# Performance work log

Hardware: AMD Instinct MI355X
Metric: run time of the kernel (lower is better)

The kernel has to match this reference:

```python
import jax, jax.numpy as jnp
import numpy as np

U, N, E, D = 200000, 50000, 1600000, 64


def setup_inputs() -> dict:
    key = jax.random.key(0)
    ks = jax.random.split(key, 8)
    nodes = jax.random.randint(ks[0], (N,), 0, U)
    neigh_idx = jax.random.randint(ks[1], (E,), 0, U)
    seg_ids = jnp.sort(jax.random.randint(ks[2], (E,), 0, N))
    u2e = jax.random.normal(ks[3], (U, D), dtype=jnp.float32) * 0.1
    W1 = jax.random.normal(ks[4], (2 * D, D), dtype=jnp.float32) * 0.1
    b1 = jnp.zeros((D,), dtype=jnp.float32)
    W2 = jax.random.normal(ks[5], (D, D), dtype=jnp.float32) * 0.1
    b2 = jnp.zeros((D,), dtype=jnp.float32)
    w3 = jax.random.normal(ks[6], (D, 1), dtype=jnp.float32) * 0.1
    b3 = jnp.zeros((1,), dtype=jnp.float32)
    return {"nodes": nodes, "neigh_idx": neigh_idx, "seg_ids": seg_ids,
            "u2e": u2e, "W1": W1, "b1": b1, "W2": W2, "b2": b2,
            "w3": w3, "b3": b3}


def reference(nodes, neigh_idx, seg_ids, u2e, W1, b1, W2, b2, w3, b3):
    # Per-node self representation  [N, D]
    u_rep = u2e[nodes]
    # Ragged neighbor gather flattened to edge list
    e_u = u2e[neigh_idx]                      # [E, D]
    u_edge = u_rep[seg_ids]                   # [E, D] node rep broadcast to its edges
    # Attention MLP (GraphRec-style), eval mode (no dropout)
    x = jnp.concatenate([e_u, u_edge], axis=1)            # [E, 2D]
    x = jax.nn.relu(x @ W1 + b1)
    x = jax.nn.relu(x @ W2 + b2)
    logits = (x @ w3 + b3)[:, 0]                           # [E]
    # Segment softmax over each node's neighbor set
    seg_max = jax.ops.segment_max(logits, seg_ids, num_segments=N)
    ex = jnp.exp(logits - seg_max[seg_ids])
    denom = jax.ops.segment_sum(ex, seg_ids, num_segments=N)
    att = ex / denom[seg_ids]                              # [E]
    # Attention-weighted neighbor aggregation: e_u^T @ att per node
    agg = jax.ops.segment_sum(att[:, None] * e_u, seg_ids, num_segments=N)  # [N, D]
    # Nodes with zero neighbors fall back to their own embedding
    counts = jax.ops.segment_sum(jnp.ones((E,), dtype=jnp.float32), seg_ids, num_segments=N)
    out = jnp.where(counts[:, None] > 0, agg, u_rep)
    return out
```

## Files before the change

### kernel.cpp

```cpp
#include <hip/hip_runtime.h>
#include <math.h>

#define D 64

typedef __fp16 fp16x2 __attribute__((ext_vector_type(2)));
typedef _Float16 half8 __attribute__((ext_vector_type(8)));
typedef _Float16 half4v __attribute__((ext_vector_type(4)));
typedef __attribute__((ext_vector_type(4))) float f32x4;

union h8pun { half8 v; fp16x2 h2[4]; };

__global__ __launch_bounds__(256) void k_prep(const float* __restrict__ W1,
                                              const float* __restrict__ W2,
                                              float* __restrict__ W1at,
                                              float* __restrict__ W1bt,
                                              float* __restrict__ W2pt,
                                              const int* __restrict__ seg_ids,
                                              int* __restrict__ start, int E, int N) {
    int i = blockIdx.x * 256 + threadIdx.x;
    if (i < 3 * D * D) {
        int mat = i / (D * D), j = i % (D * D);
        if (mat == 0) {
            int r = j >> 6, c = j & 63;
            W1at[c * D + r] = W1[r * D + c];
        } else if (mat == 1) {
            int r = j >> 6, c = j & 63;
            W1bt[c * D + r] = W1[(D + r) * D + c];
        } else {
            int n = j >> 6, pos = j & 63;
            int k = (pos >> 2) + 16 * (pos & 3);
            W2pt[n * D + pos] = W2[k * D + n];
        }
    }
    if (i <= N) {
        int lo = 0, hi = E;
        while (lo < hi) {
            int mid = (lo + hi) >> 1;
            if (seg_ids[mid] < i) lo = mid + 1; else hi = mid;
        }
        start[i] = lo;
    }
}

__global__ __launch_bounds__(256) void k_proj_both(const float* __restrict__ u2e,
                                                   const int* __restrict__ nodes,
                                                   const float* __restrict__ W1at,
                                                   const float* __restrict__ W1bt,
                                                   const float* __restrict__ b1,
                                                   _Float16* __restrict__ q,
                                                   _Float16* __restrict__ u2e_h,
                                                   _Float16* __restrict__ p,
                                                   int U, int N, int wavesU, int wavesN) {
    int lane = threadIdx.x & 63;
    int m = lane & 15, quad = lane >> 4;
    int wave = (blockIdx.x * blockDim.x + threadIdx.x) >> 6;

    const float* Wt;
    const int* idx;
    const float* bias;
    _Float16* outp;
    _Float16* copyp;
    int R, w0, wstride;
    if (wave < wavesU) {
        Wt = W1at; idx = nullptr; bias = nullptr; outp = q; copyp = u2e_h;
        R = U; w0 = wave; wstride = wavesU;
    } else {
        Wt = W1bt; idx = nodes; bias = b1; outp = p; copyp = nullptr;
        R = N; w0 = wave - wavesU; wstride = wavesN;
    }

    half8 Bf[2][4];
    float bv[4];
#pragma unroll
    for (int t = 0; t < 4; ++t) {
        int n = m + 16 * t;
        bv[t] = bias ? bias[n] : 0.0f;
#pragma unroll
        for (int kh = 0; kh < 2; ++kh) {
            const float* col = Wt + n * D + kh * 32 + quad * 8;
#pragma unroll
            for (int j = 0; j < 8; ++j) Bf[kh][t][j] = (_Float16)col[j];
        }
    }

    int ngroups = (R + 15) / 16;
    for (int g = w0; g < ngroups; g += wstride) {
        int r_ = g * 16 + m;
        int rs = r_ < R ? r_ : R - 1;
        int src = idx ? idx[rs] : rs;
        const float4* arow = (const float4*)(u2e + (size_t)src * D);
        float4 x0 = arow[quad * 2], x1 = arow[quad * 2 + 1];
        float4 y0 = arow[8 + quad * 2], y1 = arow[8 + quad * 2 + 1];
        h8pun A0, A1;
        A0.h2[0] = __builtin_amdgcn_cvt_pkrtz(x0.x, x0.y);
        A0.h2[1] = __builtin_amdgcn_cvt_pkrtz(x0.z, x0.w);
        A0.h2[2] = __builtin_amdgcn_cvt_pkrtz(x1.x, x1.y);
        A0.h2[3] = __builtin_amdgcn_cvt_pkrtz(x1.z, x1.w);
        A1.h2[0] = __builtin_amdgcn_cvt_pkrtz(y0.x, y0.y);
        A1.h2[1] = __builtin_amdgcn_cvt_pkrtz(y0.z, y0.w);
        A1.h2[2] = __builtin_amdgcn_cvt_pkrtz(y1.x, y1.y);
        A1.h2[3] = __builtin_amdgcn_cvt_pkrtz(y1.z, y1.w);
        if (copyp && r_ < R) {
            *(half8*)(copyp + (size_t)r_ * D + quad * 8) = A0.v;
            *(half8*)(copyp + (size_t)r_ * D + 32 + quad * 8) = A1.v;
        }
        f32x4 C[4];
#pragma unroll
        for (int t = 0; t < 4; ++t) C[t] = (f32x4){bv[t], bv[t], bv[t], bv[t]};
#pragma unroll
        for (int t = 0; t < 4; ++t) {
            C[t] = __builtin_amdgcn_mfma_f32_16x16x32_f16(A0.v, Bf[0][t], C[t], 0, 0, 0);
            C[t] = __builtin_amdgcn_mfma_f32_16x16x32_f16(A1.v, Bf[1][t], C[t], 0, 0, 0);
        }
#pragma unroll
        for (int r = 0; r < 4; ++r) {
            int row = g * 16 + quad * 4 + r;
            if (row < R) {
                half4v hv = {(_Float16)C[0][r], (_Float16)C[1][r],
                             (_Float16)C[2][r], (_Float16)C[3][r]};
                *(half4v*)(outp + (size_t)row * D + m * 4) = hv;
            }
        }
    }
}

__global__ __launch_bounds__(256) void k_edge_logits_mfma(const int* __restrict__ neigh_idx,
                                                          const int* __restrict__ seg_ids,
                                                          const _Float16* __restrict__ q,
                                                          const _Float16* __restrict__ p,
                                                          const float* __restrict__ W2pt,
                                                          const float* __restrict__ b2,
                                                          const float* __restrict__ w3,
                                                          const float* __restrict__ b3,
                                                          float* __restrict__ logits, int E) {
    int lane = threadIdx.x & 63;
    int m = lane & 15, quad = lane >> 4;

    half8 Bf[2][4];
    float b2v[4], w3v[4];
#pragma unroll
    for (int t = 0; t < 4; ++t) {
        int n = m + 16 * t;
        b2v[t] = b2[n];
        w3v[t] = w3[n];
#pragma unroll
        for (int kh = 0; kh < 2; ++kh) {
            const float* col = W2pt + n * D + kh * 32 + quad * 8;
#pragma unroll
            for (int j = 0; j < 8; ++j) Bf[kh][t][j] = (_Float16)col[j];
        }
    }
    float b3v = b3[0];
    const half8 hz = {0, 0, 0, 0, 0, 0, 0, 0};

    int ngroups = (E + 31) / 32;
    int wave = (blockIdx.x * blockDim.x + threadIdx.x) >> 6;
    int nwaves = (gridDim.x * blockDim.x) >> 6;
    for (int g = wave; g < ngroups; g += nwaves) {
        int ea = g * 32 + m, eb = ea + 16;
        int eas = ea < E ? ea : E - 1;
        int ebs = eb < E ? eb : E - 1;
        int nbra = neigh_idx[eas], sega = seg_ids[eas];
        int nbrb = neigh_idx[ebs], segb = seg_ids[ebs];
        const half8* qra = (const half8*)(q + (size_t)nbra * D);
        const half8* pra = (const half8*)(p + (size_t)sega * D);
        const half8* qrb = (const half8*)(q + (size_t)nbrb * D);
        const half8* prb = (const half8*)(p + (size_t)segb * D);
        half8 qa0 = qra[quad], qa1 = qra[quad + 4];
        half8 pa0 = pra[quad], pa1 = pra[quad + 4];
        half8 qb0 = qrb[quad], qb1 = qrb[quad + 4];
        half8 pb0 = prb[quad], pb1 = prb[quad + 4];
        half8 Aa0 = __builtin_elementwise_max(qa0 + pa0, hz);
        half8 Aa1 = __builtin_elementwise_max(qa1 + pa1, hz);
        half8 Ab0 = __builtin_elementwise_max(qb0 + pb0, hz);
        half8 Ab1 = __builtin_elementwise_max(qb1 + pb1, hz);
        f32x4 Ca[4], Cb[4];
#pragma unroll
        for (int t = 0; t < 4; ++t) {
            Ca[t] = (f32x4){b2v[t], b2v[t], b2v[t], b2v[t]};
            Cb[t] = Ca[t];
        }
#pragma unroll
        for (int t = 0; t < 4; ++t) {
            Ca[t] = __builtin_amdgcn_mfma_f32_16x16x32_f16(Aa0, Bf[0][t], Ca[t], 0, 0, 0);
            Ca[t] = __builtin_amdgcn_mfma_f32_16x16x32_f16(Aa1, Bf[1][t], Ca[t], 0, 0, 0);
            Cb[t] = __builtin_amdgcn_mfma_f32_16x16x32_f16(Ab0, Bf[0][t], Cb[t], 0, 0, 0);
            Cb[t] = __builtin_amdgcn_mfma_f32_16x16x32_f16(Ab1, Bf[1][t], Cb[t], 0, 0, 0);
        }
        float pa[4], pb[4];
#pragma unroll
        for (int r = 0; r < 4; ++r) {
            float sa = 0.0f, sb = 0.0f;
#pragma unroll
            for (int t = 0; t < 4; ++t) {
                sa += fmaxf(Ca[t][r], 0.0f) * w3v[t];
                sb += fmaxf(Cb[t][r], 0.0f) * w3v[t];
            }
            pa[r] = sa; pb[r] = sb;
        }
#pragma unroll
        for (int off = 1; off <= 8; off <<= 1) {
#pragma unroll
            for (int r = 0; r < 4; ++r) {
                pa[r] += __shfl_xor(pa[r], off, 64);
                pb[r] += __shfl_xor(pb[r], off, 64);
            }
        }
        if (m == 0) {
            int e0 = g * 32 + quad * 4;
            if (e0 + 3 < E)
                *(float4*)(logits + e0) = make_float4(pa[0] + b3v, pa[1] + b3v, pa[2] + b3v, pa[3] + b3v);
            else
#pragma unroll
                for (int r = 0; r < 4; ++r)
                    if (e0 + r < E) logits[e0 + r] = pa[r] + b3v;
            int e1 = e0 + 16;
            if (e1 + 3 < E)
                *(float4*)(logits + e1) = make_float4(pb[0] + b3v, pb[1] + b3v, pb[2] + b3v, pb[3] + b3v);
            else
#pragma unroll
                for (int r = 0; r < 4; ++r)
                    if (e1 + r < E) logits[e1 + r] = pb[r] + b3v;
        }
    }
}

__global__ __launch_bounds__(256) void k_agg(const int* __restrict__ nodes,
                                             const int* __restrict__ neigh_idx,
                                             const float* __restrict__ u2e,
                                             const _Float16* __restrict__ u2e_h,
                                             const float* __restrict__ logits,
                                             const int* __restrict__ start,
                                             float* __restrict__ out, int N) {
    int n = blockIdx.x * 4 + ((int)threadIdx.x >> 6);
    int lane = threadIdx.x & 63;
    if (n >= N) return;
    int s = start[n];
    int t = start[n + 1];
    if (s == t) {
        int node = nodes[n];
        out[(size_t)n * D + lane] = u2e[(size_t)node * D + lane];
        return;
    }
    float mx = -INFINITY;
    for (int i = s + lane; i < t; i += 64) mx = fmaxf(mx, logits[i]);
#pragma unroll
    for (int off = 32; off >= 1; off >>= 1) mx = fmaxf(mx, __shfl_xor(mx, off, 64));
    float ssum = 0.0f;
    for (int i = s + lane; i < t; i += 64) ssum += __expf(logits[i] - mx);
#pragma unroll
    for (int off = 32; off >= 1; off >>= 1) ssum += __shfl_xor(ssum, off, 64);
    float inv = 1.0f / ssum;

    int grp = lane >> 3, sub = lane & 7;
    float acc[8];
#pragma unroll
    for (int j = 0; j < 8; ++j) acc[j] = 0.0f;
    for (int i = s; i < t; i += 32) {
#pragma unroll
        for (int uu = 0; uu < 4; ++uu) {
            int ii = i + uu * 8 + grp;
            bool v = ii < t;
            int is = v ? ii : s;
            float lg = logits[is];
            int nb = neigh_idx[is];
            half8 r = *(const half8*)(u2e_h + (size_t)nb * D + sub * 8);
            float a = v ? __expf(lg - mx) * inv : 0.0f;
#pragma unroll
            for (int j = 0; j < 8; ++j) acc[j] += a * (float)r[j];
        }
    }
#pragma unroll
    for (int off = 8; off <= 32; off <<= 1) {
#pragma unroll
        for (int j = 0; j < 8; ++j) acc[j] += __shfl_xor(acc[j], off, 64);
    }
    if (grp == 0) {
        float* o = out + (size_t)n * D + sub * 8;
        *(float4*)o = make_float4(acc[0], acc[1], acc[2], acc[3]);
        *(float4*)(o + 4) = make_float4(acc[4], acc[5], acc[6], acc[7]);
    }
}

extern "C" void kernel_launch(void* const* d_in, const int* in_sizes, int n_in,
                              void* d_out, int out_size, void* d_ws, size_t ws_size,
                              hipStream_t stream) {
    const int* nodes = (const int*)d_in[0];
    const int* neigh_idx = (const int*)d_in[1];
    const int* seg_ids = (const int*)d_in[2];
    const float* u2e = (const float*)d_in[3];
    const float* W1 = (const float*)d_in[4];
    const float* b1 = (const float*)d_in[5];
    const float* W2 = (const float*)d_in[6];
    const float* b2 = (const float*)d_in[7];
    const float* w3 = (const float*)d_in[8];
    const float* b3 = (const float*)d_in[9];
    float* out = (float*)d_out;

    int N = in_sizes[0];
    int E = in_sizes[1];
    int U = in_sizes[3] / D;

    char* ws = (char*)d_ws;
    size_t off = 0;
    auto alloc = [&](size_t bytes) {
        void* ptr = ws + off;
        off = (off + bytes + 255) & ~(size_t)255;
        return ptr;
    };
    float* logits = (float*)alloc((size_t)E * 4);
    int* start = (int*)alloc((size_t)(N + 1) * 4);
    float* W1at = (float*)alloc((size_t)D * D * 4);
    float* W1bt = (float*)alloc((size_t)D * D * 4);
    float* W2pt = (float*)alloc((size_t)D * D * 4);
    _Float16* q = (_Float16*)alloc((size_t)U * D * 2);
    _Float16* p = (_Float16*)alloc((size_t)N * D * 2);
    _Float16* u2e_h = (_Float16*)alloc((size_t)U * D * 2);
    (void)ws_size;

    int prep_n = (N + 1) > 3 * D * D ? (N + 1) : 3 * D * D;
    k_prep<<<(prep_n + 255) / 256, 256, 0, stream>>>(W1, W2, W1at, W1bt, W2pt,
                                                     seg_ids, start, E, N);
    const int wavesU = 4096, wavesN = 1024;
    k_proj_both<<<(wavesU + wavesN) / 4, 256, 0, stream>>>(u2e, nodes, W1at, W1bt, b1,
                                                           q, u2e_h, p, U, N, wavesU, wavesN);
    k_edge_logits_mfma<<<2048, 256, 0, stream>>>(neigh_idx, seg_ids, q, p, W2pt,
                                                 b2, w3, b3, logits, E);
    k_agg<<<(N + 3) / 4, 256, 0, stream>>>(nodes, neigh_idx, u2e, u2e_h, logits, start, out, N);
}
```

Before: 238.5 us.

## Restructure edge-logit kernel to iterate per segment using CSR start offsets

The edge MLP kernel now assigns each wave one node segment at a time, using the CSR start array. It loads that node's projected row p once per segment and processes the segment's edges in chunks of 16, instead of streaming flat 32-edge groups that read seg_ids for every edge. This removes the per-edge seg_ids read and the repeated p-row gathers. In exchange, partially filled 16-edge chunks at segment tails waste MFMA and load work, each iteration has half the independent work (16 edges instead of 32), and load balance now depends on segment sizes.

```diff
diff --git a/kernel.cpp b/kernel.cpp
--- a/kernel.cpp
+++ b/kernel.cpp
@@ -124,15 +124,15 @@
     }
 }
 
-__global__ __launch_bounds__(256) void k_edge_logits_mfma(const int* __restrict__ neigh_idx,
-                                                          const int* __restrict__ seg_ids,
-                                                          const _Float16* __restrict__ q,
-                                                          const _Float16* __restrict__ p,
-                                                          const float* __restrict__ W2pt,
-                                                          const float* __restrict__ b2,
-                                                          const float* __restrict__ w3,
-                                                          const float* __restrict__ b3,
-                                                          float* __restrict__ logits, int E) {
+__global__ __launch_bounds__(256) void k_edge_seg(const int* __restrict__ neigh_idx,
+                                                  const _Float16* __restrict__ q,
+                                                  const _Float16* __restrict__ p,
+                                                  const float* __restrict__ W2pt,
+                                                  const float* __restrict__ b2,
+                                                  const float* __restrict__ w3,
+                                                  const float* __restrict__ b3,
+                                                  const int* __restrict__ start,
+                                                  float* __restrict__ logits, int N) {
     int lane = threadIdx.x & 63;
     int m = lane & 15, quad = lane >> 4;
 
@@ -153,74 +153,55 @@
     float b3v = b3[0];
     const half8 hz = {0, 0, 0, 0, 0, 0, 0, 0};
 
-    int ngroups = (E + 31) / 32;
     int wave = (blockIdx.x * blockDim.x + threadIdx.x) >> 6;
     int nwaves = (gridDim.x * blockDim.x) >> 6;
-    for (int g = wave; g < ngroups; g += nwaves) {
-        int ea = g * 32 + m, eb = ea + 16;
-        int eas = ea < E ? ea : E - 1;
-        int ebs = eb < E ? eb : E - 1;
-        int nbra = neigh_idx[eas], sega = seg_ids[eas];
-        int nbrb = neigh_idx[ebs], segb = seg_ids[ebs];
-        const half8* qra = (const half8*)(q + (size_t)nbra * D);
-        const half8* pra = (const half8*)(p + (size_t)sega * D);
-        const half8* qrb = (const half8*)(q + (size_t)nbrb * D);
-        const half8* prb = (const half8*)(p + (size_t)segb * D);
-        half8 qa0 = qra[quad], qa1 = qra[quad + 4];
-        half8 pa0 = pra[quad], pa1 = pra[quad + 4];
-        half8 qb0 = qrb[quad], qb1 = qrb[quad + 4];
-        half8 pb0 = prb[quad], pb1 = prb[quad + 4];
-        half8 Aa0 = __builtin_elementwise_max(qa0 + pa0, hz);
-        half8 Aa1 = __builtin_elementwise_max(qa1 + pa1, hz);
-        half8 Ab0 = __builtin_elementwise_max(qb0 + pb0, hz);
-        half8 Ab1 = __builtin_elementwise_max(qb1 + pb1, hz);
-        f32x4 Ca[4], Cb[4];
-#pragma unroll
-        for (int t = 0; t < 4; ++t) {
-            Ca[t] = (f32x4){b2v[t], b2v[t], b2v[t], b2v[t]};
-            Cb[t] = Ca[t];
-        }
-#pragma unroll
-        for (int t = 0; t < 4; ++t) {
-            Ca[t] = __builtin_amdgcn_mfma_f32_16x16x32_f16(Aa0, Bf[0][t], Ca[t], 0, 0, 0);
-            Ca[t] = __builtin_amdgcn_mfma_f32_16x16x32_f16(Aa1, Bf[1][t], Ca[t], 0, 0, 0);
-            Cb[t] = __builtin_amdgcn_mfma_f32_16x16x32_f16(Ab0, Bf[0][t], Cb[t], 0, 0, 0);
-            Cb[t] = __builtin_amdgcn_mfma_f32_16x16x32_f16(Ab1, Bf[1][t], Cb[t], 0, 0, 0);
-        }
-        float pa[4], pb[4];
-#pragma unroll
-        for (int r = 0; r < 4; ++r) {
-            float sa = 0.0f, sb = 0.0f;
-#pragma unroll
-            for (int t = 0; t < 4; ++t) {
-                sa += fmaxf(Ca[t][r], 0.0f) * w3v[t];
-                sb += fmaxf(Cb[t][r], 0.0f) * w3v[t];
-            }
-            pa[r] = sa; pb[r] = sb;
-        }
-#pragma unroll
-        for (int off = 1; off <= 8; off <<= 1) {
+    for (int n = wave; n < N; n += nwaves) {
+        int s = start[n], t = start[n + 1];
+        if (s >= t) continue;
+        const half8* prow = (const half8*)(p + (size_t)n * D);
+        half8 pa0 = prow[quad], pa1 = prow[quad + 4];
+        for (int base = s; base < t; base += 16) {
+            int e = base + m;
+            int es = e < t ? e : t - 1;
+            int nb = neigh_idx[es];
+            const half8* qrow = (const half8*)(q + (size_t)nb * D);
+            half8 qa0 = qrow[quad], qa1 = qrow[quad + 4];
+            half8 A0 = __builtin_elementwise_max(qa0 + pa0, hz);
+            half8 A1 = __builtin_elementwise_max(qa1 + pa1, hz);
+            f32x4 C[4];
+#pragma unroll
+            for (int t4 = 0; t4 < 4; ++t4)
+                C[t4] = (f32x4){b2v[t4], b2v[t4], b2v[t4], b2v[t4]};
+#pragma unroll
+            for (int t4 = 0; t4 < 4; ++t4) {
+                C[t4] = __builtin_amdgcn_mfma_f32_16x16x32_f16(A0, Bf[0][t4], C[t4], 0, 0, 0);
+                C[t4] = __builtin_amdgcn_mfma_f32_16x16x32_f16(A1, Bf[1][t4], C[t4], 0, 0, 0);
+            }
+            float lw[4];
 #pragma unroll
             for (int r = 0; r < 4; ++r) {
-                pa[r] += __shfl_xor(pa[r], off, 64);
-                pb[r] += __shfl_xor(pb[r], off, 64);
-            }
-        }
-        if (m == 0) {
-            int e0 = g * 32 + quad * 4;
-            if (e0 + 3 < E)
-                *(float4*)(logits + e0) = make_float4(pa[0] + b3v, pa[1] + b3v, pa[2] + b3v, pa[3] + b3v);
-            else
-#pragma unroll
-                for (int r = 0; r < 4; ++r)
-                    if (e0 + r < E) logits[e0 + r] = pa[r] + b3v;
-            int e1 = e0 + 16;
-            if (e1 + 3 < E)
-                *(float4*)(logits + e1) = make_float4(pb[0] + b3v, pb[1] + b3v, pb[2] + b3v, pb[3] + b3v);
-            else
-#pragma unroll
-                for (int r = 0; r < 4; ++r)
-                    if (e1 + r < E) logits[e1 + r] = pb[r] + b3v;
+                float sa = 0.0f;
+#pragma unroll
+                for (int t4 = 0; t4 < 4; ++t4)
+                    sa += fmaxf(C[t4][r], 0.0f) * w3v[t4];
+                lw[r] = sa;
+            }
+#pragma unroll
+            for (int off = 1; off <= 8; off <<= 1) {
+#pragma unroll
+                for (int r = 0; r < 4; ++r) lw[r] += __shfl_xor(lw[r], off, 64);
+            }
+            if (m == 0) {
+                int e0 = base + quad * 4;
+                if (e0 + 3 < t) {
+                    *(float4*)(logits + e0) = make_float4(lw[0] + b3v, lw[1] + b3v,
+                                                          lw[2] + b3v, lw[3] + b3v);
+                } else {
+#pragma unroll
+                    for (int r = 0; r < 4; ++r)
+                        if (e0 + r < t) logits[e0 + r] = lw[r] + b3v;
+                }
+            }
         }
     }
 }
@@ -324,7 +305,7 @@
     const int wavesU = 4096, wavesN = 1024;
     k_proj_both<<<(wavesU + wavesN) / 4, 256, 0, stream>>>(u2e, nodes, W1at, W1bt, b1,
                                                            q, u2e_h, p, U, N, wavesU, wavesN);
-    k_edge_logits_mfma<<<2048, 256, 0, stream>>>(neigh_idx, seg_ids, q, p, W2pt,
-                                                 b2, w3, b3, logits, E);
+    k_edge_seg<<<2048, 256, 0, stream>>>(neigh_idx, q, p, W2pt, b2, w3, b3,
+                                         start, logits, N);
     k_agg<<<(N + 3) / 4, 256, 0, stream>>>(nodes, neigh_idx, u2e, u2e_h, logits, start, out, N);
 }
```

Measured after the change: 258.2 us. 8.3% more time.

## Bucket edges by neighbor index range before the edge-logit MLP for gather locality

Applied to the files above, without the earlier changes.

Adds a stable counting sort (histogram, scan, scatter) that partitions edges into 16 buckets by neighbor id range, writing permuted neighbor, segment and original-index arrays. The edge-logit kernel then reads edges in bucket order, so random q-row gathers fall within a smaller slice of the table at a time and should hit cache more often. Logits are scattered back through the original index. The cost is two extra kernel launches, about 20 MB of extra index traffic, and scalar scattered logit stores in place of float4 stores. The edge grid is also halved.

```diff
diff --git a/kernel.cpp b/kernel.cpp
--- a/kernel.cpp
+++ b/kernel.cpp
@@ -2,6 +2,8 @@
 #include <math.h>
 
 #define D 64
+#define NBK 16
+#define SORT_BLOCKS 512
 
 typedef __fp16 fp16x2 __attribute__((ext_vector_type(2)));
 typedef _Float16 half8 __attribute__((ext_vector_type(8)));
@@ -9,6 +11,10 @@
 typedef __attribute__((ext_vector_type(4))) float f32x4;
 
 union h8pun { half8 v; fp16x2 h2[4]; };
+
+__device__ inline int bkey(int nb, int U) {
+    return (int)(((unsigned long long)nb * NBK) / (unsigned)U);
+}
 
 __global__ __launch_bounds__(256) void k_prep(const float* __restrict__ W1,
                                               const float* __restrict__ W2,
@@ -16,29 +22,120 @@
                                               float* __restrict__ W1bt,
                                               float* __restrict__ W2pt,
                                               const int* __restrict__ seg_ids,
-                                              int* __restrict__ start, int E, int N) {
-    int i = blockIdx.x * 256 + threadIdx.x;
-    if (i < 3 * D * D) {
-        int mat = i / (D * D), j = i % (D * D);
-        if (mat == 0) {
-            int r = j >> 6, c = j & 63;
-            W1at[c * D + r] = W1[r * D + c];
-        } else if (mat == 1) {
-            int r = j >> 6, c = j & 63;
-            W1bt[c * D + r] = W1[(D + r) * D + c];
-        } else {
-            int n = j >> 6, pos = j & 63;
-            int k = (pos >> 2) + 16 * (pos & 3);
-            W2pt[n * D + pos] = W2[k * D + n];
-        }
-    }
-    if (i <= N) {
-        int lo = 0, hi = E;
-        while (lo < hi) {
-            int mid = (lo + hi) >> 1;
-            if (seg_ids[mid] < i) lo = mid + 1; else hi = mid;
-        }
-        start[i] = lo;
+                                              int* __restrict__ start,
+                                              const int* __restrict__ neigh_idx,
+                                              int* __restrict__ blockhist,
+                                              int E, int N, int U, int PB, int chunk) {
+    int tid = threadIdx.x;
+    if ((int)blockIdx.x < PB) {
+        int i = blockIdx.x * 256 + tid;
+        if (i < 3 * D * D) {
+            int mat = i / (D * D), j = i % (D * D);
+            if (mat == 0) {
+                int r = j >> 6, c = j & 63;
+                W1at[c * D + r] = W1[r * D + c];
+            } else if (mat == 1) {
+                int r = j >> 6, c = j & 63;
+                W1bt[c * D + r] = W1[(D + r) * D + c];
+            } else {
+                int n = j >> 6, pos = j & 63;
+                int k = (pos >> 2) + 16 * (pos & 3);
+                W2pt[n * D + pos] = W2[k * D + n];
+            }
+        }
+        if (i <= N) {
+            int lo = 0, hi = E;
+            while (lo < hi) {
+                int mid = (lo + hi) >> 1;
+                if (seg_ids[mid] < i) lo = mid + 1; else hi = mid;
+            }
+            start[i] = lo;
+        }
+    } else {
+        int b = blockIdx.x - PB;
+        __shared__ int lcnt[NBK];
+        if (tid < NBK) lcnt[tid] = 0;
+        __syncthreads();
+        int lo = b * chunk, hi = lo + chunk; if (hi > E) hi = E;
+        for (int i = lo + tid; i < hi; i += 256)
+            atomicAdd(&lcnt[bkey(neigh_idx[i], U)], 1);
+        __syncthreads();
+        if (tid < NBK) blockhist[b * NBK + tid] = lcnt[tid];
+    }
+}
+
+__global__ __launch_bounds__(256) void k_scan(const int* __restrict__ blockhist,
+                                              int* __restrict__ baseout) {
+    __shared__ int part[NBK][NBK];
+    __shared__ int tot[NBK];
+    __shared__ int bbase[NBK];
+    int tid = threadIdx.x;
+    int k = tid & 15, j = tid >> 4;
+    int s = 0;
+    for (int i = j * 32; i < j * 32 + 32; ++i) s += blockhist[i * NBK + k];
+    part[k][j] = s;
+    __syncthreads();
+    if (tid < NBK) {
+        int run = 0;
+        for (int j2 = 0; j2 < NBK; ++j2) { int v = part[tid][j2]; part[tid][j2] = run; run += v; }
+        tot[tid] = run;
+    }
+    __syncthreads();
+    if (tid == 0) {
+        int run = 0;
+        for (int k2 = 0; k2 < NBK; ++k2) { bbase[k2] = run; run += tot[k2]; }
+    }
+    __syncthreads();
+    int running = bbase[k] + part[k][j];
+    for (int i = j * 32; i < j * 32 + 32; ++i) {
+        baseout[i * NBK + k] = running;
+        running += blockhist[i * NBK + k];
+    }
+}
+
+__global__ __launch_bounds__(256) void k_scatter(const int* __restrict__ neigh_idx,
+                                                 const int* __restrict__ seg_ids,
+                                                 const int* __restrict__ baseout,
+                                                 int* __restrict__ enb,
+                                                 int* __restrict__ eseg,
+                                                 int* __restrict__ eorg,
+                                                 int E, int U, int chunk) {
+    __shared__ int ofs[NBK];
+    __shared__ int wcnt[4][NBK];
+    int tid = threadIdx.x;
+    int b = blockIdx.x;
+    int w = tid >> 6, lane = tid & 63;
+    if (tid < NBK) ofs[tid] = baseout[b * NBK + tid];
+    __syncthreads();
+    int lo = b * chunk, hi = lo + chunk; if (hi > E) hi = E;
+    for (int base = lo; base < hi; base += 256) {
+        int i = base + tid;
+        bool v = i < hi;
+        int nb = 0, key = 0;
+        if (v) { nb = neigh_idx[i]; key = bkey(nb, U); }
+        int myrank = 0;
+        for (int k2 = 0; k2 < NBK; ++k2) {
+            unsigned long long bal = __ballot(v && key == k2);
+            if (v && key == k2)
+                myrank = __popcll(bal & ((1ull << lane) - 1ull));
+            if (lane == 0) wcnt[w][k2] = __popcll(bal);
+        }
+        __syncthreads();
+        if (v) {
+            int pre = 0;
+            for (int w2 = 0; w2 < w; ++w2) pre += wcnt[w2][key];
+            int pos = ofs[key] + pre + myrank;
+            enb[pos] = nb;
+            eseg[pos] = seg_ids[i];
+            eorg[pos] = i;
+        }
+        __syncthreads();
+        if (tid < NBK) {
+            int t = 0;
+            for (int w2 = 0; w2 < 4; ++w2) t += wcnt[w2][tid];
+            ofs[tid] += t;
+        }
+        __syncthreads();
     }
 }
 
@@ -124,15 +221,16 @@
     }
 }
 
-__global__ __launch_bounds__(256) void k_edge_logits_mfma(const int* __restrict__ neigh_idx,
-                                                          const int* __restrict__ seg_ids,
-                                                          const _Float16* __restrict__ q,
-                                                          const _Float16* __restrict__ p,
-                                                          const float* __restrict__ W2pt,
-                                                          const float* __restrict__ b2,
-                                                          const float* __restrict__ w3,
-                                                          const float* __restrict__ b3,
-                                                          float* __restrict__ logits, int E) {
+__global__ __launch_bounds__(256) void k_edge_bucket(const int* __restrict__ enb,
+                                                     const int* __restrict__ eseg,
+                                                     const int* __restrict__ eorg,
+                                                     const _Float16* __restrict__ q,
+                                                     const _Float16* __restrict__ p,
+                                                     const float* __restrict__ W2pt,
+                                                     const float* __restrict__ b2,
+                                                     const float* __restrict__ w3,
+                                                     const float* __restrict__ b3,
+                                                     float* __restrict__ logits, int E) {
     int lane = threadIdx.x & 63;
     int m = lane & 15, quad = lane >> 4;
 
@@ -160,8 +258,8 @@
         int ea = g * 32 + m, eb = ea + 16;
         int eas = ea < E ? ea : E - 1;
         int ebs = eb < E ? eb : E - 1;
-        int nbra = neigh_idx[eas], sega = seg_ids[eas];
-        int nbrb = neigh_idx[ebs], segb = seg_ids[ebs];
+        int nbra = enb[eas], sega = eseg[eas];
+        int nbrb = enb[ebs], segb = eseg[ebs];
         const half8* qra = (const half8*)(q + (size_t)nbra * D);
         const half8* pra = (const half8*)(p + (size_t)sega * D);
         const half8* qrb = (const half8*)(q + (size_t)nbrb * D);
@@ -208,19 +306,13 @@
         }
         if (m == 0) {
             int e0 = g * 32 + quad * 4;
-            if (e0 + 3 < E)
-                *(float4*)(logits + e0) = make_float4(pa[0] + b3v, pa[1] + b3v, pa[2] + b3v, pa[3] + b3v);
-            else
-#pragma unroll
-                for (int r = 0; r < 4; ++r)
-                    if (e0 + r < E) logits[e0 + r] = pa[r] + b3v;
+#pragma unroll
+            for (int r = 0; r < 4; ++r)
+                if (e0 + r < E) logits[eorg[e0 + r]] = pa[r] + b3v;
             int e1 = e0 + 16;
-            if (e1 + 3 < E)
-                *(float4*)(logits + e1) = make_float4(pb[0] + b3v, pb[1] + b3v, pb[2] + b3v, pb[3] + b3v);
-            else
-#pragma unroll
-                for (int r = 0; r < 4; ++r)
-                    if (e1 + r < E) logits[e1 + r] = pb[r] + b3v;
+#pragma unroll
+            for (int r = 0; r < 4; ++r)
+                if (e1 + r < E) logits[eorg[e1 + r]] = pb[r] + b3v;
         }
     }
 }
@@ -316,15 +408,27 @@
     _Float16* q = (_Float16*)alloc((size_t)U * D * 2);
     _Float16* p = (_Float16*)alloc((size_t)N * D * 2);
     _Float16* u2e_h = (_Float16*)alloc((size_t)U * D * 2);
+    int* blockhist = (int*)alloc((size_t)SORT_BLOCKS * NBK * 4);
+    int* baseout = (int*)alloc((size_t)SORT_BLOCKS * NBK * 4);
+    int* enb = (int*)alloc((size_t)E * 4);
+    int* eseg = (int*)alloc((size_t)E * 4);
+    int* eorg = (int*)alloc((size_t)E * 4);
     (void)ws_size;
 
-    int prep_n = (N + 1) > 3 * D * D ? (N + 1) : 3 * D * D;
-    k_prep<<<(prep_n + 255) / 256, 256, 0, stream>>>(W1, W2, W1at, W1bt, W2pt,
-                                                     seg_ids, start, E, N);
+    int chunk = (E + SORT_BLOCKS - 1) / SORT_BLOCKS;
+    int prep_work = (N + 1) > 3 * D * D ? (N + 1) : 3 * D * D;
+    int PB = (prep_work + 255) / 256;
+
+    k_prep<<<PB + SORT_BLOCKS, 256, 0, stream>>>(W1, W2, W1at, W1bt, W2pt,
+                                                 seg_ids, start, neigh_idx, blockhist,
+                                                 E, N, U, PB, chunk);
+    k_scan<<<1, 256, 0, stream>>>(blockhist, baseout);
+    k_scatter<<<SORT_BLOCKS, 256, 0, stream>>>(neigh_idx, seg_ids, baseout,
+                                               enb, eseg, eorg, E, U, chunk);
     const int wavesU = 4096, wavesN = 1024;
     k_proj_both<<<(wavesU + wavesN) / 4, 256, 0, stream>>>(u2e, nodes, W1at, W1bt, b1,
                                                            q, u2e_h, p, U, N, wavesU, wavesN);
-    k_edge_logits_mfma<<<2048, 256, 0, stream>>>(neigh_idx, seg_ids, q, p, W2pt,
-                                                 b2, w3, b3, logits, E);
+    k_edge_bucket<<<1024, 256, 0, stream>>>(enb, eseg, eorg, q, p, W2pt,
+                                            b2, w3, b3, logits, E);
     k_agg<<<(N + 3) / 4, 256, 0, stream>>>(nodes, neigh_idx, u2e, u2e_h, logits, start, out, N);
 }
```

Result: slower. 296.2 us (+24.2%).
